# Kernel tuning notes

Hardware: AMD Instinct MI355X
Metric: run time of the kernel (lower is better)

Reference implementation:

```python
import jax, jax.numpy as jnp
import numpy as np

N = 2048
TAU = 1.0  # torch gumbel_softmax default tau


def _st_binary(p, g):
    # Faithful to torch.nn.functional.gumbel_softmax(hard=True) applied to
    # logits stack((p, 1-p)), returning the class-0 indicator with
    # straight-through gradients through the soft sample.
    z0 = p + g[..., 0]
    z1 = (1.0 - p) + g[..., 1]
    soft = jax.nn.sigmoid((z0 - z1) / TAU)  # softmax over 2 classes, class 0
    hard = (z0 > z1).astype(p.dtype)
    return jax.lax.stop_gradient(hard - soft) + soft


def setup_inputs() -> dict:
    key = jax.random.key(0)
    k1, k2, k3, k4 = jax.random.split(key, 4)
    return {
        "root_probs": jax.random.uniform(k1, (N,), dtype=jnp.float32),
        "edge_probs": jax.random.uniform(k2, (N, N), dtype=jnp.float32),
        "g_root": jax.random.gumbel(k3, (N, 2), dtype=jnp.float32),
        "g_edge": jax.random.gumbel(k4, (N, N, 2), dtype=jnp.float32),
    }


def reference(root_probs, edge_probs, g_root, g_edge):
    n = root_probs.shape[0]
    roots = _st_binary(root_probs, g_root)      # (n,) hard 0/1 root indicators
    samples = _st_binary(edge_probs, g_edge)    # (n, n) hard 0/1 edge samples
    not_root = 1.0 - roots                      # (n,)
    idx = jnp.arange(n)

    # Carry anc: (n, n) with anc[j, k] = dag[k, j] for rows k already processed,
    # i.e. anc[i] is the direct-parent indicator of node i (its 'ancestors' minus i).
    def step(anc, xs):
        i, s_row = xs
        anc_i = anc[i]                                   # parents of i so far
        onehot_i = (idx == i).astype(s_row.dtype)
        # Original zeroes candidates by constant assignment -> detached mask.
        mask = jax.lax.stop_gradient((1.0 - anc_i) * (1.0 - onehot_i))
        row = s_row * not_root * mask                    # dag row i
        # ancestors[j].add(i) iff dag[i, j] == 1 (set update is non-differentiable)
        anc = anc.at[:, i].set(jax.lax.stop_gradient(row))
        return anc, row

    anc0 = jnp.zeros((n, n), dtype=samples.dtype)
    _, dag = jax.lax.scan(step, anc0, (idx, samples))
    return dag
```

## Files before the change

### kernel.cpp

```cpp
#include <hip/hip_runtime.h>


constexpr int TS = 32;

__global__ __launch_bounds__(256) void dag_kernel(
    const float*  __restrict__ rp,
    const float*  __restrict__ ep,
    const float2* __restrict__ gr,
    const float4* __restrict__ ge4,
    float* __restrict__ out, int n)
{
    __shared__ float Ash[TS][TS + 1];
    __shared__ float nrA[TS];
    __shared__ float nrB[TS];

    int p = blockIdx.x;
    int a = (int)((sqrtf(8.0f * (float)p + 1.0f) - 1.0f) * 0.5f);
    while ((a + 1) * (a + 2) / 2 <= p) ++a;
    while (a * (a + 1) / 2 > p) --a;
    const int bi = p - a * (a + 1) / 2;
    const int bj = a;
    const int I = bi * TS, J = bj * TS;

    const int t   = threadIdx.x;
    const int row = t >> 3;
    const int c4  = (t & 7) << 2;

    if (t < TS) {
        int j = J + t;
        float pj = rp[j]; float2 g = gr[j];
        nrA[t] = ((pj + g.x) > ((1.0f - pj) + g.y)) ? 0.0f : 1.0f;
    } else if (t < 2 * TS) {
        int j = I + (t - TS);
        float pj = rp[j]; float2 g = gr[j];
        nrB[t - TS] = ((pj + g.x) > ((1.0f - pj) + g.y)) ? 0.0f : 1.0f;
    }
    __syncthreads();

    const size_t idxA = (size_t)(I + row) * n + (size_t)(J + c4);
    float4 epv = *(const float4*)(ep + idxA);
    float4 q0  = ge4[idxA >> 1];
    float4 q1  = ge4[(idxA >> 1) + 1];
    float av[4];
    av[0] = ((epv.x + q0.x) > ((1.0f - epv.x) + q0.y)) ? nrA[c4 + 0] : 0.0f;
    av[1] = ((epv.y + q0.z) > ((1.0f - epv.y) + q0.w)) ? nrA[c4 + 1] : 0.0f;
    av[2] = ((epv.z + q1.x) > ((1.0f - epv.z) + q1.y)) ? nrA[c4 + 2] : 0.0f;
    av[3] = ((epv.w + q1.z) > ((1.0f - epv.w) + q1.w)) ? nrA[c4 + 3] : 0.0f;
    Ash[row][c4 + 0] = av[0];
    Ash[row][c4 + 1] = av[1];
    Ash[row][c4 + 2] = av[2];
    Ash[row][c4 + 3] = av[3];

    if (bi == bj) {
        __syncthreads();
        float4 v;
        float* vp = &v.x;
#pragma unroll
        for (int c = 0; c < 4; ++c) {
            int col = c4 + c;
            if (row == col)      vp[c] = 0.0f;
            else if (row < col)  vp[c] = av[c];
            else                 vp[c] = av[c] * (1.0f - Ash[col][row]);
        }
        *(float4*)(out + idxA) = v;
    } else {
        *(float4*)(out + idxA) = make_float4(av[0], av[1], av[2], av[3]);

        const size_t idxB = (size_t)(J + row) * n + (size_t)(I + c4);
        float4 epb = *(const float4*)(ep + idxB);
        float4 r0  = ge4[idxB >> 1];
        float4 r1  = ge4[(idxB >> 1) + 1];
        float bv[4];
        bv[0] = ((epb.x + r0.x) > ((1.0f - epb.x) + r0.y)) ? nrB[c4 + 0] : 0.0f;
        bv[1] = ((epb.y + r0.z) > ((1.0f - epb.y) + r0.w)) ? nrB[c4 + 1] : 0.0f;
        bv[2] = ((epb.z + r1.x) > ((1.0f - epb.z) + r1.y)) ? nrB[c4 + 2] : 0.0f;
        bv[3] = ((epb.w + r1.z) > ((1.0f - epb.w) + r1.w)) ? nrB[c4 + 3] : 0.0f;

        __syncthreads();
        float4 w;
        w.x = bv[0] * (1.0f - Ash[c4 + 0][row]);
        w.y = bv[1] * (1.0f - Ash[c4 + 1][row]);
        w.z = bv[2] * (1.0f - Ash[c4 + 2][row]);
        w.w = bv[3] * (1.0f - Ash[c4 + 3][row]);
        *(float4*)(out + idxB) = w;
    }
}

extern "C" void kernel_launch(void* const* d_in, const int* in_sizes, int n_in,
                              void* d_out, int out_size, void* d_ws, size_t ws_size,
                              hipStream_t stream) {
    const float*  rp = (const float*)d_in[0];
    const float*  ep = (const float*)d_in[1];
    const float2* gr = (const float2*)d_in[2];
    const float4* ge = (const float4*)d_in[3];
    float* out = (float*)d_out;
    const int n = in_sizes[0];

    const int nb = n / TS;
    const int pairs = nb * (nb + 1) / 2;
    dag_kernel<<<pairs, 256, 0, stream>>>(rp, ep, gr, ge, out, n);
}
```

Measured before the change: 15.63 us.

## Issue all tile loads upfront with nontemporal hints and compute root masks per thread

Hoists the B-tile global loads (edge probs and gumbel noise) to the start of the kernel so they are in flight alongside the A-tile loads. Uses nontemporal loads and stores for the streamed edge, noise and output data. Replaces the shared-memory root-mask stage and its barrier with each thread recomputing its own four root indicators from vectorized loads. This adds some redundant root loads and compute and raises register pressure, in exchange for more memory-level parallelism and one fewer sync.

```diff
diff --git a/kernel.cpp b/kernel.cpp
--- a/kernel.cpp
+++ b/kernel.cpp
@@ -1,18 +1,18 @@
 #include <hip/hip_runtime.h>
 
+
+typedef float f4 __attribute__((ext_vector_type(4)));
 
 constexpr int TS = 32;
 
 __global__ __launch_bounds__(256) void dag_kernel(
-    const float*  __restrict__ rp,
-    const float*  __restrict__ ep,
-    const float2* __restrict__ gr,
-    const float4* __restrict__ ge4,
+    const float* __restrict__ rp,
+    const f4*    __restrict__ gr4,
+    const float* __restrict__ ep,
+    const f4*    __restrict__ ge4,
     float* __restrict__ out, int n)
 {
     __shared__ float Ash[TS][TS + 1];
-    __shared__ float nrA[TS];
-    __shared__ float nrB[TS];
 
     int p = blockIdx.x;
     int a = (int)((sqrtf(8.0f * (float)p + 1.0f) - 1.0f) * 0.5f);
@@ -21,82 +21,97 @@
     const int bi = p - a * (a + 1) / 2;
     const int bj = a;
     const int I = bi * TS, J = bj * TS;
+    const bool diag = (bi == bj);
 
     const int t   = threadIdx.x;
     const int row = t >> 3;
     const int c4  = (t & 7) << 2;
 
-    if (t < TS) {
-        int j = J + t;
-        float pj = rp[j]; float2 g = gr[j];
-        nrA[t] = ((pj + g.x) > ((1.0f - pj) + g.y)) ? 0.0f : 1.0f;
-    } else if (t < 2 * TS) {
-        int j = I + (t - TS);
-        float pj = rp[j]; float2 g = gr[j];
-        nrB[t - TS] = ((pj + g.x) > ((1.0f - pj) + g.y)) ? 0.0f : 1.0f;
+    const size_t idxA = (size_t)(I + row) * n + (size_t)(J + c4);
+    const size_t idxB = (size_t)(J + row) * n + (size_t)(I + c4);
+
+    const f4 epA = __builtin_nontemporal_load((const f4*)(ep + idxA));
+    const f4 qA0 = __builtin_nontemporal_load(ge4 + (idxA >> 1));
+    const f4 qA1 = __builtin_nontemporal_load(ge4 + (idxA >> 1) + 1);
+    f4 epB, qB0, qB1;
+    if (!diag) {
+        epB = __builtin_nontemporal_load((const f4*)(ep + idxB));
+        qB0 = __builtin_nontemporal_load(ge4 + (idxB >> 1));
+        qB1 = __builtin_nontemporal_load(ge4 + (idxB >> 1) + 1);
     }
-    __syncthreads();
 
-    const size_t idxA = (size_t)(I + row) * n + (size_t)(J + c4);
-    float4 epv = *(const float4*)(ep + idxA);
-    float4 q0  = ge4[idxA >> 1];
-    float4 q1  = ge4[(idxA >> 1) + 1];
+    const f4 rpA = *(const f4*)(rp + J + c4);
+    const f4 gA0 = gr4[(J + c4) >> 1];
+    const f4 gA1 = gr4[((J + c4) >> 1) + 1];
+    float nA[4];
+    nA[0] = ((rpA.x + gA0.x) > ((1.0f - rpA.x) + gA0.y)) ? 0.0f : 1.0f;
+    nA[1] = ((rpA.y + gA0.z) > ((1.0f - rpA.y) + gA0.w)) ? 0.0f : 1.0f;
+    nA[2] = ((rpA.z + gA1.x) > ((1.0f - rpA.z) + gA1.y)) ? 0.0f : 1.0f;
+    nA[3] = ((rpA.w + gA1.z) > ((1.0f - rpA.w) + gA1.w)) ? 0.0f : 1.0f;
+
     float av[4];
-    av[0] = ((epv.x + q0.x) > ((1.0f - epv.x) + q0.y)) ? nrA[c4 + 0] : 0.0f;
-    av[1] = ((epv.y + q0.z) > ((1.0f - epv.y) + q0.w)) ? nrA[c4 + 1] : 0.0f;
-    av[2] = ((epv.z + q1.x) > ((1.0f - epv.z) + q1.y)) ? nrA[c4 + 2] : 0.0f;
-    av[3] = ((epv.w + q1.z) > ((1.0f - epv.w) + q1.w)) ? nrA[c4 + 3] : 0.0f;
+    av[0] = ((epA.x + qA0.x) > ((1.0f - epA.x) + qA0.y)) ? nA[0] : 0.0f;
+    av[1] = ((epA.y + qA0.z) > ((1.0f - epA.y) + qA0.w)) ? nA[1] : 0.0f;
+    av[2] = ((epA.z + qA1.x) > ((1.0f - epA.z) + qA1.y)) ? nA[2] : 0.0f;
+    av[3] = ((epA.w + qA1.z) > ((1.0f - epA.w) + qA1.w)) ? nA[3] : 0.0f;
     Ash[row][c4 + 0] = av[0];
     Ash[row][c4 + 1] = av[1];
     Ash[row][c4 + 2] = av[2];
     Ash[row][c4 + 3] = av[3];
 
-    if (bi == bj) {
+    if (diag) {
         __syncthreads();
-        float4 v;
-        float* vp = &v.x;
+        f4 v;
 #pragma unroll
         for (int c = 0; c < 4; ++c) {
             int col = c4 + c;
-            if (row == col)      vp[c] = 0.0f;
-            else if (row < col)  vp[c] = av[c];
-            else                 vp[c] = av[c] * (1.0f - Ash[col][row]);
+            float x;
+            if (row == col)      x = 0.0f;
+            else if (row < col)  x = av[c];
+            else                 x = av[c] * (1.0f - Ash[col][row]);
+            v[c] = x;
         }
-        *(float4*)(out + idxA) = v;
+        __builtin_nontemporal_store(v, (f4*)(out + idxA));
     } else {
-        *(float4*)(out + idxA) = make_float4(av[0], av[1], av[2], av[3]);
+        f4 u = {av[0], av[1], av[2], av[3]};
+        __builtin_nontemporal_store(u, (f4*)(out + idxA));
 
-        const size_t idxB = (size_t)(J + row) * n + (size_t)(I + c4);
-        float4 epb = *(const float4*)(ep + idxB);
-        float4 r0  = ge4[idxB >> 1];
-        float4 r1  = ge4[(idxB >> 1) + 1];
+        const f4 rpB = *(const f4*)(rp + I + c4);
+        const f4 gB0 = gr4[(I + c4) >> 1];
+        const f4 gB1 = gr4[((I + c4) >> 1) + 1];
+        float nB[4];
+        nB[0] = ((rpB.x + gB0.x) > ((1.0f - rpB.x) + gB0.y)) ? 0.0f : 1.0f;
+        nB[1] = ((rpB.y + gB0.z) > ((1.0f - rpB.y) + gB0.w)) ? 0.0f : 1.0f;
+        nB[2] = ((rpB.z + gB1.x) > ((1.0f - rpB.z) + gB1.y)) ? 0.0f : 1.0f;
+        nB[3] = ((rpB.w + gB1.z) > ((1.0f - rpB.w) + gB1.w)) ? 0.0f : 1.0f;
+
         float bv[4];
-        bv[0] = ((epb.x + r0.x) > ((1.0f - epb.x) + r0.y)) ? nrB[c4 + 0] : 0.0f;
-        bv[1] = ((epb.y + r0.z) > ((1.0f - epb.y) + r0.w)) ? nrB[c4 + 1] : 0.0f;
-        bv[2] = ((epb.z + r1.x) > ((1.0f - epb.z) + r1.y)) ? nrB[c4 + 2] : 0.0f;
-        bv[3] = ((epb.w + r1.z) > ((1.0f - epb.w) + r1.w)) ? nrB[c4 + 3] : 0.0f;
+        bv[0] = ((epB.x + qB0.x) > ((1.0f - epB.x) + qB0.y)) ? nB[0] : 0.0f;
+        bv[1] = ((epB.y + qB0.z) > ((1.0f - epB.y) + qB0.w)) ? nB[1] : 0.0f;
+        bv[2] = ((epB.z + qB1.x) > ((1.0f - epB.z) + qB1.y)) ? nB[2] : 0.0f;
+        bv[3] = ((epB.w + qB1.z) > ((1.0f - epB.w) + qB1.w)) ? nB[3] : 0.0f;
 
         __syncthreads();
-        float4 w;
+        f4 w;
         w.x = bv[0] * (1.0f - Ash[c4 + 0][row]);
         w.y = bv[1] * (1.0f - Ash[c4 + 1][row]);
         w.z = bv[2] * (1.0f - Ash[c4 + 2][row]);
         w.w = bv[3] * (1.0f - Ash[c4 + 3][row]);
-        *(float4*)(out + idxB) = w;
+        __builtin_nontemporal_store(w, (f4*)(out + idxB));
     }
 }
 
 extern "C" void kernel_launch(void* const* d_in, const int* in_sizes, int n_in,
                               void* d_out, int out_size, void* d_ws, size_t ws_size,
                               hipStream_t stream) {
-    const float*  rp = (const float*)d_in[0];
-    const float*  ep = (const float*)d_in[1];
-    const float2* gr = (const float2*)d_in[2];
-    const float4* ge = (const float4*)d_in[3];
+    const float* rp = (const float*)d_in[0];
+    const float* ep = (const float*)d_in[1];
+    const f4*    gr = (const f4*)d_in[2];
+    const f4*    ge = (const f4*)d_in[3];
     float* out = (float*)d_out;
     const int n = in_sizes[0];
 
     const int nb = n / TS;
     const int pairs = nb * (nb + 1) / 2;
-    dag_kernel<<<pairs, 256, 0, stream>>>(rp, ep, gr, ge, out, n);
+    dag_kernel<<<pairs, 256, 0, stream>>>(rp, gr, ep, ge, out, n);
 }
```

After: 16.41 us. 4.9% more time.

## Enlarge tile to 64 and hoist all global loads before the sync

Applied to the files above, without the earlier changes.

The tile size goes from 32 to 64. Each thread now handles four rows and issues all of its edge-probability and Gumbel loads for both the A and B tiles up front, ahead of the root-mask computation and the barrier. This is meant to raise memory-level parallelism and hide load latency, and the A-tile shared store now holds the raw sample with the root mask applied later. In exchange the block count drops by about four times, which may leave the GPU underoccupied, and register pressure goes up.

```diff
diff --git a/kernel.cpp b/kernel.cpp
--- a/kernel.cpp
+++ b/kernel.cpp
@@ -1,18 +1,20 @@
 #include <hip/hip_runtime.h>
 
 
-constexpr int TS = 32;
+typedef float f4 __attribute__((ext_vector_type(4)));
+
+constexpr int TS = 64;
 
 __global__ __launch_bounds__(256) void dag_kernel(
     const float*  __restrict__ rp,
+    const float2* __restrict__ gr2,
     const float*  __restrict__ ep,
-    const float2* __restrict__ gr,
-    const float4* __restrict__ ge4,
+    const f4*     __restrict__ ge4,
     float* __restrict__ out, int n)
 {
     __shared__ float Ash[TS][TS + 1];
-    __shared__ float nrA[TS];
-    __shared__ float nrB[TS];
+    __shared__ float nrJ[TS];
+    __shared__ float nrI[TS];
 
     int p = blockIdx.x;
     int a = (int)((sqrtf(8.0f * (float)p + 1.0f) - 1.0f) * 0.5f);
@@ -21,68 +23,108 @@
     const int bi = p - a * (a + 1) / 2;
     const int bj = a;
     const int I = bi * TS, J = bj * TS;
+    const bool diag = (bi == bj);
 
-    const int t   = threadIdx.x;
-    const int row = t >> 3;
-    const int c4  = (t & 7) << 2;
+    const int t  = threadIdx.x;
+    const int r0 = t >> 4;
+    const int c4 = (t & 15) << 2;
+
+    f4 epA[4], qA0[4], qA1[4];
+#pragma unroll
+    for (int r = 0; r < 4; ++r) {
+        size_t idx = (size_t)(I + r0 + r * 16) * n + (size_t)(J + c4);
+        epA[r] = *(const f4*)(ep + idx);
+        qA0[r] = ge4[idx >> 1];
+        qA1[r] = ge4[(idx >> 1) + 1];
+    }
+    f4 epB[4], qB0[4], qB1[4];
+    if (!diag) {
+#pragma unroll
+        for (int r = 0; r < 4; ++r) {
+            size_t idx = (size_t)(J + r0 + r * 16) * n + (size_t)(I + c4);
+            epB[r] = *(const f4*)(ep + idx);
+            qB0[r] = ge4[idx >> 1];
+            qB1[r] = ge4[(idx >> 1) + 1];
+        }
+    }
 
     if (t < TS) {
         int j = J + t;
-        float pj = rp[j]; float2 g = gr[j];
-        nrA[t] = ((pj + g.x) > ((1.0f - pj) + g.y)) ? 0.0f : 1.0f;
+        float pj = rp[j]; float2 g = gr2[j];
+        nrJ[t] = ((pj + g.x) > ((1.0f - pj) + g.y)) ? 0.0f : 1.0f;
     } else if (t < 2 * TS) {
         int j = I + (t - TS);
-        float pj = rp[j]; float2 g = gr[j];
-        nrB[t - TS] = ((pj + g.x) > ((1.0f - pj) + g.y)) ? 0.0f : 1.0f;
+        float pj = rp[j]; float2 g = gr2[j];
+        nrI[t - TS] = ((pj + g.x) > ((1.0f - pj) + g.y)) ? 0.0f : 1.0f;
     }
+
+    float sA[4][4];
+#pragma unroll
+    for (int r = 0; r < 4; ++r) {
+        int row = r0 + r * 16;
+        sA[r][0] = ((epA[r].x + qA0[r].x) > ((1.0f - epA[r].x) + qA0[r].y)) ? 1.0f : 0.0f;
+        sA[r][1] = ((epA[r].y + qA0[r].z) > ((1.0f - epA[r].y) + qA0[r].w)) ? 1.0f : 0.0f;
+        sA[r][2] = ((epA[r].z + qA1[r].x) > ((1.0f - epA[r].z) + qA1[r].y)) ? 1.0f : 0.0f;
+        sA[r][3] = ((epA[r].w + qA1[r].z) > ((1.0f - epA[r].w) + qA1[r].w)) ? 1.0f : 0.0f;
+        Ash[row][c4 + 0] = sA[r][0];
+        Ash[row][c4 + 1] = sA[r][1];
+        Ash[row][c4 + 2] = sA[r][2];
+        Ash[row][c4 + 3] = sA[r][3];
+    }
+
+    float sB[4][4];
+    if (!diag) {
+#pragma unroll
+        for (int r = 0; r < 4; ++r) {
+            sB[r][0] = ((epB[r].x + qB0[r].x) > ((1.0f - epB[r].x) + qB0[r].y)) ? 1.0f : 0.0f;
+            sB[r][1] = ((epB[r].y + qB0[r].z) > ((1.0f - epB[r].y) + qB0[r].w)) ? 1.0f : 0.0f;
+            sB[r][2] = ((epB[r].z + qB1[r].x) > ((1.0f - epB[r].z) + qB1[r].y)) ? 1.0f : 0.0f;
+            sB[r][3] = ((epB[r].w + qB1[r].z) > ((1.0f - epB[r].w) + qB1[r].w)) ? 1.0f : 0.0f;
+        }
+    }
+
     __syncthreads();
 
-    const size_t idxA = (size_t)(I + row) * n + (size_t)(J + c4);
-    float4 epv = *(const float4*)(ep + idxA);
-    float4 q0  = ge4[idxA >> 1];
-    float4 q1  = ge4[(idxA >> 1) + 1];
-    float av[4];
-    av[0] = ((epv.x + q0.x) > ((1.0f - epv.x) + q0.y)) ? nrA[c4 + 0] : 0.0f;
-    av[1] = ((epv.y + q0.z) > ((1.0f - epv.y) + q0.w)) ? nrA[c4 + 1] : 0.0f;
-    av[2] = ((epv.z + q1.x) > ((1.0f - epv.z) + q1.y)) ? nrA[c4 + 2] : 0.0f;
-    av[3] = ((epv.w + q1.z) > ((1.0f - epv.w) + q1.w)) ? nrA[c4 + 3] : 0.0f;
-    Ash[row][c4 + 0] = av[0];
-    Ash[row][c4 + 1] = av[1];
-    Ash[row][c4 + 2] = av[2];
-    Ash[row][c4 + 3] = av[3];
+    if (diag) {
+#pragma unroll
+        for (int r = 0; r < 4; ++r) {
+            int row = r0 + r * 16;
+            size_t idx = (size_t)(I + row) * n + (size_t)(J + c4);
+            float nr_row = nrJ[row];
+            f4 v;
+#pragma unroll
+            for (int c = 0; c < 4; ++c) {
+                int col = c4 + c;
+                float x;
+                if (row == col)      x = 0.0f;
+                else if (row < col)  x = sA[r][c] * nrJ[col];
+                else                 x = sA[r][c] * nrJ[col] *
+                                         (1.0f - Ash[col][row] * nr_row);
+                v[c] = x;
+            }
+            *(f4*)(out + idx) = v;
+        }
+    } else {
+#pragma unroll
+        for (int r = 0; r < 4; ++r) {
+            int row = r0 + r * 16;
+            size_t idxA = (size_t)(I + row) * n + (size_t)(J + c4);
+            f4 u;
+            u.x = sA[r][0] * nrJ[c4 + 0];
+            u.y = sA[r][1] * nrJ[c4 + 1];
+            u.z = sA[r][2] * nrJ[c4 + 2];
+            u.w = sA[r][3] * nrJ[c4 + 3];
+            *(f4*)(out + idxA) = u;
 
-    if (bi == bj) {
-        __syncthreads();
-        float4 v;
-        float* vp = &v.x;
-#pragma unroll
-        for (int c = 0; c < 4; ++c) {
-            int col = c4 + c;
-            if (row == col)      vp[c] = 0.0f;
-            else if (row < col)  vp[c] = av[c];
-            else                 vp[c] = av[c] * (1.0f - Ash[col][row]);
+            size_t idxB = (size_t)(J + row) * n + (size_t)(I + c4);
+            float nr_row = nrJ[row];
+            f4 w;
+            w.x = sB[r][0] * nrI[c4 + 0] * (1.0f - Ash[c4 + 0][row] * nr_row);
+            w.y = sB[r][1] * nrI[c4 + 1] * (1.0f - Ash[c4 + 1][row] * nr_row);
+            w.z = sB[r][2] * nrI[c4 + 2] * (1.0f - Ash[c4 + 2][row] * nr_row);
+            w.w = sB[r][3] * nrI[c4 + 3] * (1.0f - Ash[c4 + 3][row] * nr_row);
+            *(f4*)(out + idxB) = w;
         }
-        *(float4*)(out + idxA) = v;
-    } else {
-        *(float4*)(out + idxA) = make_float4(av[0], av[1], av[2], av[3]);
-
-        const size_t idxB = (size_t)(J + row) * n + (size_t)(I + c4);
-        float4 epb = *(const float4*)(ep + idxB);
-        float4 r0  = ge4[idxB >> 1];
-        float4 r1  = ge4[(idxB >> 1) + 1];
-        float bv[4];
-        bv[0] = ((epb.x + r0.x) > ((1.0f - epb.x) + r0.y)) ? nrB[c4 + 0] : 0.0f;
-        bv[1] = ((epb.y + r0.z) > ((1.0f - epb.y) + r0.w)) ? nrB[c4 + 1] : 0.0f;
-        bv[2] = ((epb.z + r1.x) > ((1.0f - epb.z) + r1.y)) ? nrB[c4 + 2] : 0.0f;
-        bv[3] = ((epb.w + r1.z) > ((1.0f - epb.w) + r1.w)) ? nrB[c4 + 3] : 0.0f;
-
-        __syncthreads();
-        float4 w;
-        w.x = bv[0] * (1.0f - Ash[c4 + 0][row]);
-        w.y = bv[1] * (1.0f - Ash[c4 + 1][row]);
-        w.z = bv[2] * (1.0f - Ash[c4 + 2][row]);
-        w.w = bv[3] * (1.0f - Ash[c4 + 3][row]);
-        *(float4*)(out + idxB) = w;
     }
 }
 
@@ -92,11 +134,11 @@
     const float*  rp = (const float*)d_in[0];
     const float*  ep = (const float*)d_in[1];
     const float2* gr = (const float2*)d_in[2];
-    const float4* ge = (const float4*)d_in[3];
+    const f4*     ge = (const f4*)d_in[3];
     float* out = (float*)d_out;
     const int n = in_sizes[0];
 
     const int nb = n / TS;
     const int pairs = nb * (nb + 1) / 2;
-    dag_kernel<<<pairs, 256, 0, stream>>>(rp, ep, gr, ge, out, n);
+    dag_kernel<<<pairs, 256, 0, stream>>>(rp, gr, ep, ge, out, n);
 }
```

Measured after the change: 16.70 us. 6.8% more time.
